# Optimization experiments

Measured on AMD Instinct MI355X. Metric: run time of the kernel, lower is better.

Reference implementation:

```python
import jax, jax.numpy as jnp
import numpy as np
import math

B, T, C, H, D = 2, 2048, 768, 12, 64


def _rms_norm(x):
    # torch F.rms_norm with eps=None -> finfo(dtype).eps, no learned weight
    eps = jnp.finfo(x.dtype).eps
    return x * jax.lax.rsqrt(jnp.mean(x * x, axis=-1, keepdims=True) + eps)


def _apply_rotary(x, cos, sin):
    # nanochat rotary: split head_dim into halves
    d = x.shape[-1] // 2
    x1, x2 = x[..., :d], x[..., d:]
    return jnp.concatenate([x1 * cos + x2 * sin, -x1 * sin + x2 * cos], axis=-1)


def setup_inputs() -> dict:
    key = jax.random.key(0)
    ks = jax.random.split(key, 8)
    s = 0.02
    x = jax.random.normal(ks[0], (B, T, C), jnp.float32)
    cos = jax.random.normal(ks[1], (1, T, 1, D // 2), jnp.float32)
    sin = jax.random.normal(ks[2], (1, T, 1, D // 2), jnp.float32)
    Wq = jax.random.normal(ks[3], (C, C), jnp.float32) * s
    Wk = jax.random.normal(ks[4], (C, C), jnp.float32) * s
    Wv = jax.random.normal(ks[5], (C, C), jnp.float32) * s
    Wo = jax.random.normal(ks[6], (C, C), jnp.float32) * s
    beta = jnp.ones((H,), jnp.float32) * 0.5
    return {"x": x, "cos": cos, "sin": sin, "Wq": Wq, "Wk": Wk, "Wv": Wv, "Wo": Wo, "beta": beta}


def reference(x, cos, sin, Wq, Wk, Wv, Wo, beta):
    b, t, c = x.shape
    h = beta.shape[0]
    d = c // h
    q = (x @ Wq.T).reshape(b, t, h, d)
    k = (x @ Wk.T).reshape(b, t, h, d)
    v = (x @ Wv.T).reshape(b, t, h, d)
    q = _rms_norm(_apply_rotary(q, cos, sin)).transpose(0, 2, 1, 3)  # (B,H,T,D)
    k = _rms_norm(_apply_rotary(k, cos, sin)).transpose(0, 2, 1, 3)
    v = v.transpose(0, 2, 1, 3)
    # phase coherence: mean over RoPE frequencies of cos(position_diff * theta)
    pos = jnp.arange(t, dtype=jnp.float32)
    theta = 10000.0 ** (-jnp.arange(0, d, 2, dtype=jnp.float32) / d)  # (D/2,)
    pdiff = pos[None, :] - pos[:, None]  # (T,T); cos is even so orientation is irrelevant
    coh_base = jnp.mean(jnp.cos(pdiff[:, :, None] * theta), axis=-1)  # (T,T)
    coherence = 1.0 + beta[None, :, None, None] * coh_base[None, None, :, :]  # (1,H,T,T)
    scores = jnp.einsum('bhqd,bhkd->bhqk', q, k) / math.sqrt(d)
    scores = scores * coherence
    w = jax.nn.softmax(scores, axis=-1)
    causal = jnp.tril(jnp.ones((t, t), dtype=bool))
    w = w * causal[None, None, :, :]
    w = w / (jnp.sum(w, axis=-1, keepdims=True) + 1e-8)
    y = jnp.einsum('bhqk,bhkd->bhqd', w, v)
    y = y.transpose(0, 2, 1, 3).reshape(b, t, c)
    return y @ Wo.T
```

## Files before the change

### kernel.cpp

```cpp
#include <hip/hip_runtime.h>
#include <hip/hip_bf16.h>
#include <math.h>

#define B_ 2
#define T_ 2048
#define C_ 768
#define H_ 12
#define D_ 64

typedef __attribute__((ext_vector_type(8))) short short8;
typedef __attribute__((ext_vector_type(4))) float f32x4;
typedef __attribute__((ext_vector_type(16))) float f32x16;

template <bool V> struct BoolC { static constexpr bool value = V; };

#define SBAR() do { asm volatile("" ::: "memory"); __builtin_amdgcn_s_barrier(); asm volatile("" ::: "memory"); } while (0)
#define WAITVM(N) asm volatile("s_waitcnt vmcnt(" #N ")" ::: "memory")

__device__ inline unsigned short f2bf(float f) {
    unsigned int x = __float_as_uint(f);
    unsigned int r = x + 0x7FFFu + ((x >> 16) & 1u);
    return (unsigned short)(r >> 16);
}

__device__ __forceinline__ unsigned cvtpk(float lo, float hi) {
    unsigned r;
    asm("v_cvt_pk_bf16_f32 %0, %1, %2" : "=v"(r) : "v"(lo), "v"(hi));
    return r;
}

__device__ __forceinline__ void plswap(unsigned& a, unsigned& b) {
    asm volatile("v_permlane32_swap_b32 %0, %1" : "+v"(a), "+v"(b));
}

__device__ __forceinline__ void gll16(const void* g, void* l) {
    __builtin_amdgcn_global_load_lds(
        (const __attribute__((address_space(1))) unsigned int*)g,
        (__attribute__((address_space(3))) unsigned int*)l, 16, 0, 0);
}

__global__ __launch_bounds__(256) void convert_all_kernel(const float* __restrict__ x,
                                                          const float* __restrict__ Wq,
                                                          const float* __restrict__ Wk,
                                                          const float* __restrict__ Wv,
                                                          const float* __restrict__ Wo,
                                                          unsigned short* __restrict__ xb,
                                                          unsigned short* __restrict__ wqkv,
                                                          unsigned short* __restrict__ wob,
                                                          float* __restrict__ coh) {
    if (blockIdx.x >= 5376) {
        int dd = (blockIdx.x - 5376) * 256 + threadIdx.x;
        if (dd < T_) {
            float s = 0.f;
            for (int m = 0; m < 32; ++m) {
                float theta = powf(10000.f, -(float)m / 32.f);
                s += cosf((float)dd * theta);
            }
            coh[dd] = s * (1.f / 32.f);
        }
        return;
    }
    int i = blockIdx.x * 256 + threadIdx.x;
    float4 v;
    ushort4* d;
    if (i < 786432) {
        v = ((const float4*)x)[i];
        d = (ushort4*)xb + i;
    } else {
        int wI = i - 786432;
        int widx = wI / 147456;
        int off = wI - widx * 147456;
        const float* W = widx == 0 ? Wq : widx == 1 ? Wk : widx == 2 ? Wv : Wo;
        v = ((const float4*)W)[off];
        unsigned short* base = (widx == 3) ? wob : (wqkv + widx * 589824);
        d = (ushort4*)base + off;
    }
    ushort4 o;
    o.x = f2bf(v.x); o.y = f2bf(v.y); o.z = f2bf(v.z); o.w = f2bf(v.w);
    *d = o;
}

union QkvSmem {
    struct { unsigned short A[3][128][32]; unsigned short Bm[3][64][32]; } g;
    unsigned short tr[64][136];
};

__global__ __launch_bounds__(256, 4) void gemm_qkv_kernel(const unsigned short* __restrict__ xb,
                                                          const unsigned short* __restrict__ wqkv,
                                                          const float* __restrict__ cosb,
                                                          const float* __restrict__ sinb,
                                                          unsigned short* __restrict__ qbf,
                                                          unsigned short* __restrict__ kbf,
                                                          unsigned short* __restrict__ vt) {
    __shared__ QkvSmem sm;

    int bm = blockIdx.x, tn = blockIdx.y;
    int tid = threadIdx.x;
    int w = tid >> 6, lane = tid & 63;
    int rc = lane & 15, kg = lane >> 4;

    const unsigned short* ga = xb + (size_t)(bm * 128 + w * 32 + (lane >> 2)) * 768 + (lane & 3) * 8;
    const unsigned short* gb = wqkv + (size_t)(tn * 64 + w * 16 + (lane >> 2)) * 768 + (lane & 3) * 8;

    f32x4 acc[2][4];
    #pragma unroll
    for (int i = 0; i < 2; ++i)
        #pragma unroll
        for (int j = 0; j < 4; ++j) acc[i][j] = (f32x4){0.f, 0.f, 0.f, 0.f};

    auto stageg = [&](int buf, int k0) {
        gll16(ga + k0, &sm.g.A[buf][w * 32][0]);
        gll16(ga + k0 + 16 * 768, &sm.g.A[buf][w * 32 + 16][0]);
        gll16(gb + k0, &sm.g.Bm[buf][w * 16][0]);
    };
    auto comp = [&](int buf) {
        short8 aF[2], bF[4];
        #pragma unroll
        for (int ai = 0; ai < 2; ++ai) aF[ai] = *(const short8*)&sm.g.A[buf][w * 32 + ai * 16 + rc][kg * 8];
        #pragma unroll
        for (int bj = 0; bj < 4; ++bj) bF[bj] = *(const short8*)&sm.g.Bm[buf][bj * 16 + rc][kg * 8];
        __builtin_amdgcn_s_setprio(1);
        #pragma unroll
        for (int ai = 0; ai < 2; ++ai)
            #pragma unroll
            for (int bj = 0; bj < 4; ++bj)
                acc[ai][bj] = __builtin_amdgcn_mfma_f32_16x16x32_bf16(aF[ai], bF[bj], acc[ai][bj], 0, 0, 0);
        __builtin_amdgcn_s_setprio(0);
    };

    stageg(0, 0);
    stageg(1, 32);
    __syncthreads();
    for (int kk = 0; kk < 22; ++kk) {
        stageg((kk + 2) % 3, (kk + 2) * 32);
        WAITVM(6);
        SBAR();
        comp(kk % 3);
        SBAR();
    }
    WAITVM(3);
    SBAR();
    comp(1);
    SBAR();
    WAITVM(0);
    SBAR();
    comp(2);
    __syncthreads();

    int tensor = tn / 12;
    int h = tn % 12;

    if (tensor < 2) {
        float scale = tensor == 0 ? 0.125f : 1.0f;
        unsigned short* dst = (tensor == 0 ? qbf : kbf);
        #pragma unroll
        for (int ai = 0; ai < 2; ++ai) {
            #pragma unroll
            for (int rr = 0; rr < 4; ++rr) {
                int m = bm * 128 + w * 32 + ai * 16 + kg * 4 + rr;
                int b = m >> 11, t = m & 2047;
                float c0 = cosb[t * 32 + rc], c1 = cosb[t * 32 + 16 + rc];
                float s0 = sinb[t * 32 + rc], s1 = sinb[t * 32 + 16 + rc];
                float x0 = acc[ai][0][rr], x1 = acc[ai][1][rr];
                float x2 = acc[ai][2][rr], x3 = acc[ai][3][rr];
                float o0 = x0 * c0 + x2 * s0;
                float o1 = x1 * c1 + x3 * s1;
                float o2 = -x0 * s0 + x2 * c0;
                float o3 = -x1 * s1 + x3 * c1;
                float ss = o0 * o0 + o1 * o1 + o2 * o2 + o3 * o3;
                ss += __shfl_xor(ss, 1); ss += __shfl_xor(ss, 2);
                ss += __shfl_xor(ss, 4); ss += __shfl_xor(ss, 8);
                float rn = rsqrtf(ss * (1.f / 64.f) + 1.1920929e-07f) * scale;
                unsigned short* dp = dst + (((size_t)b * H_ + h) * T_ + t) * 64;
                dp[rc]      = f2bf(o0 * rn);
                dp[16 + rc] = f2bf(o1 * rn);
                dp[32 + rc] = f2bf(o2 * rn);
                dp[48 + rc] = f2bf(o3 * rn);
            }
        }
    } else {
        #pragma unroll
        for (int ai = 0; ai < 2; ++ai)
            #pragma unroll
            for (int bj = 0; bj < 4; ++bj)
                #pragma unroll
                for (int rr = 0; rr < 4; ++rr)
                    sm.tr[bj * 16 + rc][w * 32 + ai * 16 + kg * 4 + rr] = f2bf(acc[ai][bj][rr]);
        __syncthreads();
        int m0 = bm * 128;
        int b = m0 >> 11, t0 = m0 & 2047;
        int d = w * 16 + (lane >> 2);
        int tl = (lane & 3) * 32;
        unsigned short* gp = vt + (((size_t)b * H_ + h) * 64 + d) * T_ + t0 + tl;
        #pragma unroll
        for (int i = 0; i < 4; ++i)
            *(uint4*)(gp + i * 8) = *(const uint4*)&sm.tr[d][tl + i * 8];
    }
}

__global__ __launch_bounds__(256, 4) void gemm_out_kernel(const unsigned short* __restrict__ A,
                                                          const unsigned short* __restrict__ Bw,
                                                          float* __restrict__ C) {
    __shared__ unsigned short lA[2][64][32];
    __shared__ unsigned short lB[2][64][32];
    int bm = blockIdx.x, tn = blockIdx.y;
    int tid = threadIdx.x;
    int w = tid >> 6, lane = tid & 63;
    int rc = lane & 15, kg = lane >> 4;
    int wr = w >> 1, wc = w & 1;

    const unsigned short* ga = A + (size_t)(bm * 64 + w * 16 + (lane >> 2)) * 768 + (lane & 3) * 8;
    const unsigned short* gbB = Bw + (size_t)(tn * 64 + w * 16 + (lane >> 2)) * 768 + (lane & 3) * 8;

    f32x4 acc[2][2];
    #pragma unroll
    for (int i = 0; i < 2; ++i)
        #pragma unroll
        for (int j = 0; j < 2; ++j) acc[i][j] = (f32x4){0.f, 0.f, 0.f, 0.f};

    auto stageg = [&](int buf, int k0) {
        gll16(ga + k0, &lA[buf][w * 16][0]);
        gll16(gbB + k0, &lB[buf][w * 16][0]);
    };
    auto comp = [&](int buf) {
        short8 aF[2], bF[2];
        #pragma unroll
        for (int ai = 0; ai < 2; ++ai) aF[ai] = *(const short8*)&lA[buf][wr * 32 + ai * 16 + rc][kg * 8];
        #pragma unroll
        for (int bj = 0; bj < 2; ++bj) bF[bj] = *(const short8*)&lB[buf][wc * 32 + bj * 16 + rc][kg * 8];
        __builtin_amdgcn_s_setprio(1);
        #pragma unroll
        for (int ai = 0; ai < 2; ++ai)
            #pragma unroll
            for (int bj = 0; bj < 2; ++bj)
                acc[ai][bj] = __builtin_amdgcn_mfma_f32_16x16x32_bf16(aF[ai], bF[bj], acc[ai][bj], 0, 0, 0);
        __builtin_amdgcn_s_setprio(0);
    };

    stageg(0, 0);
    __syncthreads();
    for (int kk = 0; kk < 23; ++kk) {
        stageg((kk + 1) & 1, (kk + 1) * 32);
        WAITVM(2);
        SBAR();
        comp(kk & 1);
        SBAR();
    }
    WAITVM(0);
    SBAR();
    comp(1);

    #pragma unroll
    for (int ai = 0; ai < 2; ++ai)
        #pragma unroll
        for (int rr = 0; rr < 4; ++rr) {
            int m = bm * 64 + wr * 32 + ai * 16 + kg * 4 + rr;
            #pragma unroll
            for (int bj = 0; bj < 2; ++bj)
                C[(size_t)m * 768 + tn * 64 + wc * 32 + bj * 16 + rc] = acc[ai][bj][rr];
        }
}

__global__ __launch_bounds__(256, 4) void attn_flash_kernel(const unsigned short* __restrict__ qbf,
                                                            const unsigned short* __restrict__ kbf,
                                                            const unsigned short* __restrict__ vt,
                                                            const float* __restrict__ coh,
                                                            const float* __restrict__ beta,
                                                            unsigned short* __restrict__ yb) {
    __shared__ unsigned short kT[2][64][64];
    __shared__ unsigned short vT[2][64][64];
    __shared__ float cfl[T_];

    int p = blockIdx.x;
    int xcd = p & 7, kk = p >> 3;
    int bl = kk >> 5, jsl = kk & 31;
    int bh = xcd * 3 + bl;
    int jj = (bl == 0) ? jsl : (bl == 1 ? (31 - jsl) : ((jsl * 5 + 3) & 31));
    int tq = 31 - jj;
    int b = bh / H_, h = bh % H_;

    int tid = threadIdx.x;
    int w = tid >> 6, lane = tid & 63;
    int qs = w >> 1, js = w & 1;
    int ql = lane & 31, hl = lane >> 5;

    float bv = beta[h];
    int cmax = (tq + 1) * 64;
    for (int i = tid; i < cmax; i += 256)
        cfl[i] = (1.f + bv * coh[i]) * 1.4426950408889634f;

    int qb = tq * 64;
    const unsigned short* kb = kbf + (size_t)bh * T_ * 64;
    const unsigned short* vb = vt + (size_t)bh * 64 * T_;

    const unsigned short* qrow = qbf + ((size_t)bh * T_ + qb + qs * 32 + ql) * 64 + hl * 8;
    short8 qf[4];
    #pragma unroll
    for (int d = 0; d < 4; ++d) qf[d] = *(const short8*)(qrow + d * 16);

    f32x16 acc0, acc1;
    #pragma unroll
    for (int i = 0; i < 16; ++i) { acc0[i] = 0.f; acc1[i] = 0.f; }
    float z = 0.f;

    int Rk = js * 32 + ql;
    int kby[4];
    #pragma unroll
    for (int d = 0; d < 4; ++d) kby[d] = Rk * 128 + (((d * 2 + hl) ^ (Rk & 7)) << 4);
    int vby0[2], vby1[2];
    #pragma unroll
    for (int ks = 0; ks < 2; ++ks) {
        int Rv0 = ql, Rv1 = 32 + ql;
        vby0[ks] = Rv0 * 128 + (((js * 4 + ks * 2 + hl) ^ (Rv0 & 7)) << 4);
        vby1[ks] = Rv1 * 128 + (((js * 4 + ks * 2 + hl) ^ (Rv1 & 7)) << 4);
    }
    const char* kbase = (const char*)&kT[0][0][0];
    const char* vbase = (const char*)&vT[0][0][0];

    int rloc = lane >> 3;
    int gsw = ((lane & 7) ^ rloc) * 8;
    int r0 = w * 16;

    auto stage = [&](int buf, int tj) {
        gll16(kb + (size_t)(tj + r0 + rloc) * 64 + gsw,      &kT[buf][r0][0]);
        gll16(kb + (size_t)(tj + r0 + 8 + rloc) * 64 + gsw,  &kT[buf][r0 + 8][0]);
        gll16(vb + (size_t)(r0 + rloc) * T_ + tj + gsw,      &vT[buf][r0][0]);
        gll16(vb + (size_t)(r0 + 8 + rloc) * T_ + tj + gsw,  &vT[buf][r0 + 8][0]);
    };

    int qpos = qb + qs * 32 + ql;

    auto body = [&](int buf, int tj, auto maskc) {
        constexpr bool M = decltype(maskc)::value;
        f32x16 s;
        #pragma unroll
        for (int i = 0; i < 16; ++i) s[i] = 0.f;
        const char* kp = kbase + buf * 8192;
        __builtin_amdgcn_s_setprio(1);
        #pragma unroll
        for (int d = 0; d < 4; ++d) {
            short8 kf = *(const short8*)(kp + kby[d]);
            s = __builtin_amdgcn_mfma_f32_32x32x16_bf16(kf, qf[d], s, 0, 0, 0);
        }
        __builtin_amdgcn_s_setprio(0);
        int base = qpos - tj - js * 32 - 4 * hl;
        float e[16];
        #pragma unroll
        for (int r = 0; r < 16; ++r) {
            int dd = base - ((r & 3) + 8 * (r >> 2));
            if constexpr (M) {
                float ex = __builtin_amdgcn_exp2f(s[r] * cfl[dd < 0 ? 0 : dd]);
                e[r] = dd >= 0 ? ex : 0.f;
            } else {
                e[r] = __builtin_amdgcn_exp2f(s[r] * cfl[dd]);
            }
            z += e[r];
        }
        unsigned A0 = cvtpk(e[0], e[1]),  B0 = cvtpk(e[2], e[3]);
        unsigned C0 = cvtpk(e[4], e[5]),  D0 = cvtpk(e[6], e[7]);
        unsigned E0 = cvtpk(e[8], e[9]),  F0 = cvtpk(e[10], e[11]);
        unsigned G0 = cvtpk(e[12], e[13]), H0 = cvtpk(e[14], e[15]);
        plswap(A0, C0); plswap(B0, D0); plswap(E0, G0); plswap(F0, H0);
        union U { unsigned u[4]; short8 s8; };
        U p0, p1;
        p0.u[0] = A0; p0.u[1] = B0; p0.u[2] = C0; p0.u[3] = D0;
        p1.u[0] = E0; p1.u[1] = F0; p1.u[2] = G0; p1.u[3] = H0;
        const char* vp = vbase + buf * 8192;
        short8 v00 = *(const short8*)(vp + vby0[0]);
        short8 v01 = *(const short8*)(vp + vby0[1]);
        short8 v10 = *(const short8*)(vp + vby1[0]);
        short8 v11 = *(const short8*)(vp + vby1[1]);
        __builtin_amdgcn_s_setprio(1);
        acc0 = __builtin_amdgcn_mfma_f32_32x32x16_bf16(v00, p0.s8, acc0, 0, 0, 0);
        acc0 = __builtin_amdgcn_mfma_f32_32x32x16_bf16(v01, p1.s8, acc0, 0, 0, 0);
        acc1 = __builtin_amdgcn_mfma_f32_32x32x16_bf16(v10, p0.s8, acc1, 0, 0, 0);
        acc1 = __builtin_amdgcn_mfma_f32_32x32x16_bf16(v11, p1.s8, acc1, 0, 0, 0);
        __builtin_amdgcn_s_setprio(0);
    };

    int nt = tq + 1;
    stage(0, 0);
    __syncthreads();
    int cur = 0;
    for (int it = 0; it < nt - 1; ++it) {
        stage(cur ^ 1, (it + 1) * 64);
        WAITVM(4);
        SBAR();
        body(cur, it * 64, BoolC<false>{});
        SBAR();
        cur ^= 1;
    }
    WAITVM(0);
    SBAR();
    if (qs > js)      body(cur, (nt - 1) * 64, BoolC<false>{});
    else if (qs == js) body(cur, (nt - 1) * 64, BoolC<true>{});
    __syncthreads();

    z += __shfl_xor(z, 32);
    float* osc = (float*)&kT[0][0][0];
    float* zbuf = (float*)&vT[0][0][0];
    if (js == 0) {
        float* o = osc + qs * 2048;
        #pragma unroll
        for (int r = 0; r < 16; ++r) {
            o[r * 64 + lane] = acc0[r];
            o[(16 + r) * 64 + lane] = acc1[r];
        }
        if (lane < 32) zbuf[qs * 32 + ql] = z;
    }
    __syncthreads();
    if (js == 1) {
        float zt = z + zbuf[qs * 32 + ql];
        float invz = 1.f / zt;
        const float* o = osc + qs * 2048;
        #pragma unroll
        for (int r = 0; r < 16; ++r) {
            acc0[r] = (acc0[r] + o[r * 64 + lane]) * invz;
            acc1[r] = (acc1[r] + o[(16 + r) * 64 + lane]) * invz;
        }
        int t = qb + qs * 32 + ql;
        unsigned short* yp = yb + (((size_t)b * T_ + t) * H_ + h) * 64;
        #pragma unroll
        for (int g = 0; g < 4; ++g) {
            uint2 st0, st1;
            st0.x = cvtpk(acc0[g * 4 + 0], acc0[g * 4 + 1]);
            st0.y = cvtpk(acc0[g * 4 + 2], acc0[g * 4 + 3]);
            *(uint2*)(yp + g * 8 + 4 * hl) = st0;
            st1.x = cvtpk(acc1[g * 4 + 0], acc1[g * 4 + 1]);
            st1.y = cvtpk(acc1[g * 4 + 2], acc1[g * 4 + 3]);
            *(uint2*)(yp + 32 + g * 8 + 4 * hl) = st1;
        }
    }
}

extern "C" void kernel_launch(void* const* d_in, const int* in_sizes, int n_in,
                              void* d_out, int out_size, void* d_ws, size_t ws_size,
                              hipStream_t stream) {
    const float* x    = (const float*)d_in[0];
    const float* cosb = (const float*)d_in[1];
    const float* sinb = (const float*)d_in[2];
    const float* Wq   = (const float*)d_in[3];
    const float* Wk   = (const float*)d_in[4];
    const float* Wv   = (const float*)d_in[5];
    const float* Wo   = (const float*)d_in[6];
    const float* beta = (const float*)d_in[7];
    float* out = (float*)d_out;

    char* ws = (char*)d_ws;
    unsigned short* xb   = (unsigned short*)(ws + 0);
    unsigned short* wqkv = (unsigned short*)(ws + 6291456);
    unsigned short* wob  = (unsigned short*)(ws + 9830400);
    unsigned short* qbf  = (unsigned short*)(ws + 11010048);
    unsigned short* kbf  = (unsigned short*)(ws + 17301504);
    unsigned short* vt   = (unsigned short*)(ws + 23592960);
    unsigned short* yb   = (unsigned short*)(ws + 29884416);
    float*          coh  = (float*)(ws + 36175872);

    convert_all_kernel<<<5384, 256, 0, stream>>>(x, Wq, Wk, Wv, Wo, xb, wqkv, wob, coh);

    dim3 gq(32, 36);
    gemm_qkv_kernel<<<gq, 256, 0, stream>>>(xb, wqkv, cosb, sinb, qbf, kbf, vt);

    attn_flash_kernel<<<B_ * H_ * (T_ / 64), 256, 0, stream>>>(qbf, kbf, vt, coh, beta, yb);

    dim3 go(64, 12);
    gemm_out_kernel<<<go, 256, 0, stream>>>(yb, wob, out);
}
```

Measured before the change: 97.30 us.

## Load K/V fragments directly from global memory instead of LDS double-buffering

Removes the LDS double-buffered staging of K and V tiles (async global-to-LDS loads, waitcnts and per-tile barriers) and has each wave read its MFMA operand fragments straight from global memory through the cache. The aim is to drop the per-iteration barrier synchronisation and LDS traffic. The cost is redundant global/L2 reads, since waves sharing a K/V tile each fetch it separately, and load latency that is no longer overlapped with compute by explicit prefetch. The osc and zbuf reduction buffers become dedicated shared arrays.

```diff
diff --git a/kernel.cpp b/kernel.cpp
--- a/kernel.cpp
+++ b/kernel.cpp
@@ -267,9 +267,9 @@
                                                             const float* __restrict__ coh,
                                                             const float* __restrict__ beta,
                                                             unsigned short* __restrict__ yb) {
-    __shared__ unsigned short kT[2][64][64];
-    __shared__ unsigned short vT[2][64][64];
     __shared__ float cfl[T_];
+    __shared__ float osc[4096];
+    __shared__ float zbuf[64];
 
     int p = blockIdx.x;
     int xcd = p & 7, kk = p >> 3;
@@ -304,42 +304,24 @@
     float z = 0.f;
 
     int Rk = js * 32 + ql;
-    int kby[4];
-    #pragma unroll
-    for (int d = 0; d < 4; ++d) kby[d] = Rk * 128 + (((d * 2 + hl) ^ (Rk & 7)) << 4);
-    int vby0[2], vby1[2];
-    #pragma unroll
-    for (int ks = 0; ks < 2; ++ks) {
-        int Rv0 = ql, Rv1 = 32 + ql;
-        vby0[ks] = Rv0 * 128 + (((js * 4 + ks * 2 + hl) ^ (Rv0 & 7)) << 4);
-        vby1[ks] = Rv1 * 128 + (((js * 4 + ks * 2 + hl) ^ (Rv1 & 7)) << 4);
-    }
-    const char* kbase = (const char*)&kT[0][0][0];
-    const char* vbase = (const char*)&vT[0][0][0];
-
-    int rloc = lane >> 3;
-    int gsw = ((lane & 7) ^ rloc) * 8;
-    int r0 = w * 16;
-
-    auto stage = [&](int buf, int tj) {
-        gll16(kb + (size_t)(tj + r0 + rloc) * 64 + gsw,      &kT[buf][r0][0]);
-        gll16(kb + (size_t)(tj + r0 + 8 + rloc) * 64 + gsw,  &kT[buf][r0 + 8][0]);
-        gll16(vb + (size_t)(r0 + rloc) * T_ + tj + gsw,      &vT[buf][r0][0]);
-        gll16(vb + (size_t)(r0 + 8 + rloc) * T_ + tj + gsw,  &vT[buf][r0 + 8][0]);
-    };
+    const unsigned short* kfrag = kb + (size_t)Rk * 64 + hl * 8;
+    const unsigned short* vfrag0 = vb + (size_t)ql * T_ + js * 32 + hl * 8;
+    const unsigned short* vfrag1 = vb + (size_t)(32 + ql) * T_ + js * 32 + hl * 8;
 
     int qpos = qb + qs * 32 + ql;
 
-    auto body = [&](int buf, int tj, auto maskc) {
+    __syncthreads();
+
+    auto body = [&](int tj, auto maskc) {
         constexpr bool M = decltype(maskc)::value;
         f32x16 s;
         #pragma unroll
         for (int i = 0; i < 16; ++i) s[i] = 0.f;
-        const char* kp = kbase + buf * 8192;
+        const unsigned short* kp = kfrag + (size_t)tj * 64;
         __builtin_amdgcn_s_setprio(1);
         #pragma unroll
         for (int d = 0; d < 4; ++d) {
-            short8 kf = *(const short8*)(kp + kby[d]);
+            short8 kf = *(const short8*)(kp + d * 16);
             s = __builtin_amdgcn_mfma_f32_32x32x16_bf16(kf, qf[d], s, 0, 0, 0);
         }
         __builtin_amdgcn_s_setprio(0);
@@ -365,11 +347,10 @@
         U p0, p1;
         p0.u[0] = A0; p0.u[1] = B0; p0.u[2] = C0; p0.u[3] = D0;
         p1.u[0] = E0; p1.u[1] = F0; p1.u[2] = G0; p1.u[3] = H0;
-        const char* vp = vbase + buf * 8192;
-        short8 v00 = *(const short8*)(vp + vby0[0]);
-        short8 v01 = *(const short8*)(vp + vby0[1]);
-        short8 v10 = *(const short8*)(vp + vby1[0]);
-        short8 v11 = *(const short8*)(vp + vby1[1]);
+        short8 v00 = *(const short8*)(vfrag0 + tj);
+        short8 v01 = *(const short8*)(vfrag0 + tj + 16);
+        short8 v10 = *(const short8*)(vfrag1 + tj);
+        short8 v11 = *(const short8*)(vfrag1 + tj + 16);
         __builtin_amdgcn_s_setprio(1);
         acc0 = __builtin_amdgcn_mfma_f32_32x32x16_bf16(v00, p0.s8, acc0, 0, 0, 0);
         acc0 = __builtin_amdgcn_mfma_f32_32x32x16_bf16(v01, p1.s8, acc0, 0, 0, 0);
@@ -379,26 +360,13 @@
     };
 
     int nt = tq + 1;
-    stage(0, 0);
-    __syncthreads();
-    int cur = 0;
-    for (int it = 0; it < nt - 1; ++it) {
-        stage(cur ^ 1, (it + 1) * 64);
-        WAITVM(4);
-        SBAR();
-        body(cur, it * 64, BoolC<false>{});
-        SBAR();
-        cur ^= 1;
-    }
-    WAITVM(0);
-    SBAR();
-    if (qs > js)      body(cur, (nt - 1) * 64, BoolC<false>{});
-    else if (qs == js) body(cur, (nt - 1) * 64, BoolC<true>{});
+    for (int it = 0; it < nt - 1; ++it)
+        body(it * 64, BoolC<false>{});
+    if (qs > js)       body((nt - 1) * 64, BoolC<false>{});
+    else if (qs == js) body((nt - 1) * 64, BoolC<true>{});
     __syncthreads();
 
     z += __shfl_xor(z, 32);
-    float* osc = (float*)&kT[0][0][0];
-    float* zbuf = (float*)&vT[0][0][0];
     if (js == 0) {
         float* o = osc + qs * 2048;
         #pragma unroll
```

Result: slower. 128.4 us (+32.0%).
